# Optimization experiments

Hardware: AMD Instinct MI355X
Metric: run time of the kernel (lower is better)

The kernel has to match this reference:

```python
import jax, jax.numpy as jnp
import numpy as np

B, S, D = 2, 2048, 2048
H = 1024          # per-expert swiglu hidden
E = 16            # num_experts
K = 2             # top_k
T = B * S
CAP = (K * T) // E  # capacity = top_k * tokens / experts * capacity_factor(1.0) = 512


def setup_inputs() -> dict:
    key = jax.random.key(0)
    ks = jax.random.split(key, 10)
    s = 0.02
    return {
        "hidden_states": jax.random.normal(ks[0], (B, S, D), jnp.float32),
        "gate_w": jax.random.normal(ks[1], (D, E), jnp.float32) * s,
        "w1": jax.random.normal(ks[2], (E, D, H), jnp.float32) * s,
        "w3": jax.random.normal(ks[3], (E, D, H), jnp.float32) * s,
        "w2": jax.random.normal(ks[4], (E, H, D), jnp.float32) * s,
        "sw1": jax.random.normal(ks[5], (D, H), jnp.float32) * s,
        "sw3": jax.random.normal(ks[6], (D, H), jnp.float32) * s,
        "sw2": jax.random.normal(ks[7], (H, D), jnp.float32) * s,
        "coef_w": jax.random.normal(ks[8], (D, 2), jnp.float32) * s,
        "coef_b": jnp.zeros((2,), jnp.float32),
    }


def _topk_gating(logits):
    """GShard-style top-k capacity gating. logits: [T,E] (gate runs in fp32).
    Returns combine [T,E,C], dispatch [T,E,C], l_aux scalar, exp_counts [E]."""
    probs = jax.nn.softmax(logits, axis=-1)                     # [T,E]
    top_vals, top_idx = jax.lax.top_k(probs, K)                 # [T,K]
    gates = top_vals / jnp.sum(top_vals, -1, keepdims=True)     # renormalize top-k
    masks = jax.nn.one_hot(top_idx, E, dtype=probs.dtype)       # [T,K,E]

    prior = jnp.zeros((E,), probs.dtype)
    combine = jnp.zeros((T, E, CAP), probs.dtype)
    for kk in range(K):  # fixed tiny K, structurally distinct slots
        m = masks[:, kk]                                        # [T,E]
        loc = jnp.cumsum(m, axis=0) - m + prior                 # position in expert buffer
        prior = prior + jnp.sum(m, axis=0)
        keep = m * (loc < CAP)                                  # capacity drop
        pos = jnp.sum(loc * m, axis=1).astype(jnp.int32)        # [T]
        loc_oh = jax.nn.one_hot(pos, CAP, dtype=probs.dtype)    # [T,C]
        combine = combine + gates[:, kk, None, None] * keep[:, :, None] * loc_oh[:, None, :]
    dispatch = (combine > 0).astype(probs.dtype)

    # load-balancing aux loss over top-1 assignment (GShard/DeepSpeed convention)
    me = jnp.mean(probs, axis=0)                                # [E]
    ce = jnp.mean(masks[:, 0], axis=0)                          # [E]
    l_aux = jnp.sum(me * ce) * E
    exp_counts = jnp.sum(masks, axis=(0, 1)).astype(jnp.int32)  # tokens routed per expert
    return combine, dispatch, l_aux, exp_counts


def _swiglu(x, a, b, c):
    return (jax.nn.silu(x @ a) * (x @ b)) @ c


def reference(hidden_states, gate_w, w1, w3, w2, sw1, sw3, sw2, coef_w, coef_b):
    x = hidden_states.reshape(T, D)
    logits = (x.astype(jnp.float32) @ gate_w)                   # gate kept in fp32
    combine, dispatch, l_aux, exp_counts = _topk_gating(logits)

    # dispatch -> grouped expert swiglu -> combine
    xe = jnp.einsum('tec,td->ecd', dispatch.astype(x.dtype), x)         # [E,C,D]
    h = jax.nn.silu(jnp.einsum('ecd,edh->ech', xe, w1)) * jnp.einsum('ecd,edh->ech', xe, w3)
    ye = jnp.einsum('ech,ehd->ecd', h, w2)                              # [E,C,D]
    moe_out = jnp.einsum('tec,ecd->td', combine.astype(x.dtype), ye)    # [T,D]

    # shared-expert residual MLP + softmax coefficient combine
    mlp_out = _swiglu(x, sw1, sw3, sw2)                                 # [T,D]
    coef = jax.nn.softmax(x @ coef_w + coef_b, axis=-1)                 # [T,2]
    out = moe_out * coef[:, 0:1] + mlp_out * coef[:, 1:2]
    return out.reshape(B, S, D), l_aux, exp_counts
```

## Files before the change

kernel.cpp:

```cpp
#include <hip/hip_runtime.h>
#include <hip/hip_bf16.h>
#include <stdint.h>

#define T_TOK 4096
#define DIM   2048
#define HID   1024
#define NE    16
#define CAPE  512

typedef __bf16 bf16x8 __attribute__((ext_vector_type(8)));
typedef float  f32x4  __attribute__((ext_vector_type(4)));

__device__ __forceinline__ ushort f2bf(float f) {
    union { float f; uint32_t u; } v; v.f = f;
    uint32_t r = (v.u + 0x7FFFu + ((v.u >> 16) & 1u)) >> 16;
    return (ushort)r;
}
__device__ __forceinline__ float bf2f(ushort u) {
    union { uint32_t u; float f; } v; v.u = (uint32_t)u << 16; return v.f;
}
__device__ __forceinline__ void gload16(const void* g, void* lds) {
    __builtin_amdgcn_global_load_lds(
        (const __attribute__((address_space(1))) uint32_t*)g,
        (__attribute__((address_space(3))) uint32_t*)lds, 16, 0, 0);
}
#define VMCNT(n) asm volatile("s_waitcnt vmcnt(" #n ")" ::: "memory")

__global__ __launch_bounds__(256) void logits_kernel(
    const float* __restrict__ x, const float* __restrict__ gate_w,
    const float* __restrict__ coef_w, float* __restrict__ logits,
    ushort* __restrict__ xb)
{
    __shared__ float gws[18 * 512];
    int tid = threadIdx.x;
    int wv = tid >> 6, lane = tid & 63;
    int tbase = blockIdx.x * 16 + wv * 4;
    float acc[4][18];
#pragma unroll
    for (int tk = 0; tk < 4; ++tk)
#pragma unroll
        for (int o = 0; o < 18; ++o) acc[tk][o] = 0.f;

    for (int c = 0; c < 4; ++c) {
        int d0 = c * 512;
        __syncthreads();
        const float4* g4 = (const float4*)(gate_w + (size_t)d0 * NE);
        for (int i = tid; i < 2048; i += 256) {
            float4 v = g4[i];
            int dd = i >> 2, o0 = (i & 3) * 4;
            gws[(o0 + 0) * 512 + dd] = v.x;
            gws[(o0 + 1) * 512 + dd] = v.y;
            gws[(o0 + 2) * 512 + dd] = v.z;
            gws[(o0 + 3) * 512 + dd] = v.w;
        }
        for (int i = tid; i < 1024; i += 256) {
            float v = coef_w[(size_t)d0 * 2 + i];
            gws[(16 + (i & 1)) * 512 + (i >> 1)] = v;
        }
        __syncthreads();
#pragma unroll
        for (int tk = 0; tk < 4; ++tk) {
            int t = tbase + tk;
            const float* xr = x + (size_t)t * DIM + d0;
            float xv[8];
#pragma unroll
            for (int j = 0; j < 8; ++j) xv[j] = xr[j * 64 + lane];
#pragma unroll
            for (int j = 0; j < 8; ++j)
                xb[(size_t)t * DIM + d0 + j * 64 + lane] = f2bf(xv[j]);
#pragma unroll
            for (int o = 0; o < 18; ++o) {
                const float* gr = &gws[o * 512 + lane];
                float a = acc[tk][o];
#pragma unroll
                for (int j = 0; j < 8; ++j) a += xv[j] * gr[j * 64];
                acc[tk][o] = a;
            }
        }
    }
#pragma unroll
    for (int tk = 0; tk < 4; ++tk) {
#pragma unroll
        for (int off = 32; off > 0; off >>= 1)
#pragma unroll
            for (int o = 0; o < 18; ++o)
                acc[tk][o] += __shfl_down(acc[tk][o], off, 64);
        if (lane == 0) {
#pragma unroll
            for (int o = 0; o < 18; ++o)
                logits[(size_t)(tbase + tk) * 18 + o] = acc[tk][o];
        }
    }
}

__global__ __launch_bounds__(256) void finish_kernel(
    const float* __restrict__ logits, const float* __restrict__ coef_b,
    int* __restrict__ topidx, float* __restrict__ gatesw,
    float* __restrict__ coefo, float* __restrict__ probs_sum)
{
    __shared__ float wred[4][NE];
    int t = blockIdx.x * 256 + threadIdx.x;
    float lg[18];
#pragma unroll
    for (int o = 0; o < 18; ++o) lg[o] = logits[(size_t)t * 18 + o];
    float p[NE];
    float m = lg[0];
#pragma unroll
    for (int e = 1; e < NE; ++e) m = fmaxf(m, lg[e]);
    float ssum = 0.f;
#pragma unroll
    for (int e = 0; e < NE; ++e) { p[e] = expf(lg[e] - m); ssum += p[e]; }
    float inv = 1.f / ssum;
#pragma unroll
    for (int e = 0; e < NE; ++e) p[e] *= inv;
    int i1 = 0;
#pragma unroll
    for (int e = 1; e < NE; ++e) if (p[e] > p[i1]) i1 = e;
    int i2 = -1;
#pragma unroll
    for (int e = 0; e < NE; ++e) { if (e == i1) continue; if (i2 < 0 || p[e] > p[i2]) i2 = e; }
    float g0 = p[i1], g1 = p[i2], gs = g0 + g1;
    topidx[t * 2 + 0] = i1; topidx[t * 2 + 1] = i2;
    gatesw[t * 2 + 0] = g0 / gs; gatesw[t * 2 + 1] = g1 / gs;
    float c0 = lg[16] + coef_b[0], c1 = lg[17] + coef_b[1];
    float cm = fmaxf(c0, c1);
    float e0 = expf(c0 - cm), e1 = expf(c1 - cm);
    float cs = e0 + e1;
    coefo[t * 2 + 0] = e0 / cs; coefo[t * 2 + 1] = e1 / cs;

    float r[NE];
#pragma unroll
    for (int e = 0; e < NE; ++e) r[e] = p[e];
#pragma unroll
    for (int off = 32; off > 0; off >>= 1) {
#pragma unroll
        for (int e = 0; e < NE; ++e) r[e] += __shfl_down(r[e], off, 64);
    }
    int wv = threadIdx.x >> 6, ln = threadIdx.x & 63;
    if (ln == 0) {
#pragma unroll
        for (int e = 0; e < NE; ++e) wred[wv][e] = r[e];
    }
    __syncthreads();
    if (threadIdx.x < NE) {
        float s = wred[0][threadIdx.x] + wred[1][threadIdx.x]
                + wred[2][threadIdx.x] + wred[3][threadIdx.x];
        atomicAdd(&probs_sum[threadIdx.x], s);
    }
}

__global__ __launch_bounds__(256) void scan_kernel(
    const int* __restrict__ topidx, const float* __restrict__ gatesw,
    const float* __restrict__ probs_sum,
    int* __restrict__ sidx, float* __restrict__ swt,
    int* __restrict__ assign_token, int* __restrict__ nvalid,
    float* __restrict__ out_tail)
{
    int e = blockIdx.x;
    __shared__ int wcnt[4];
    __shared__ int runs;
    __shared__ int cnt0s;
    int tid = threadIdx.x, wv = tid >> 6, ln = tid & 63;
    unsigned long long ltmask = (1ull << ln) - 1ull;
    if (tid == 0) runs = 0;
    __syncthreads();
    for (int kk = 0; kk < 2; ++kk) {
        for (int c = 0; c < T_TOK; c += 256) {
            int t = c + tid;
            bool m = (topidx[t * 2 + kk] == e);
            unsigned long long b = __ballot(m);
            int within = __popcll(b & ltmask);
            if (ln == 0) wcnt[wv] = __popcll(b);
            __syncthreads();
            int cross = 0;
            for (int w = 0; w < wv; ++w) cross += wcnt[w];
            int pos = runs + cross + within;
            if (m) {
                bool keep = pos < CAPE;
                sidx[t * 2 + kk] = keep ? (e * CAPE + pos) : -1;
                swt[t * 2 + kk] = keep ? gatesw[t * 2 + kk] : 0.f;
                if (keep) assign_token[e * CAPE + pos] = t;
            }
            __syncthreads();
            if (tid == 0) runs += wcnt[0] + wcnt[1] + wcnt[2] + wcnt[3];
            __syncthreads();
        }
        if (kk == 0 && tid == 0) cnt0s = runs;
        __syncthreads();
    }
    for (int p = runs + tid; p < CAPE; p += 256)
        assign_token[e * CAPE + p] = 0;
    if (tid == 0) {
        int total = runs;
        nvalid[e] = min(CAPE, total);
        out_tail[1 + e] = (float)total;
        float term = (probs_sum[e] / (float)T_TOK) * ((float)cnt0s / (float)T_TOK) * (float)NE;
        atomicAdd(&out_tail[0], term);
    }
}

__global__ __launch_bounds__(256) void transpose_all(
    const float* __restrict__ w1, const float* __restrict__ w3,
    const float* __restrict__ w2, const float* __restrict__ sw1,
    const float* __restrict__ sw3, const float* __restrict__ sw2,
    ushort* __restrict__ w1T, ushort* __restrict__ w3T, ushort* __restrict__ w2T,
    ushort* __restrict__ sw1T, ushort* __restrict__ sw3T, ushort* __restrict__ sw2T)
{
    __shared__ __align__(16) ushort tile[128][264];
    int id = blockIdx.x;
    const float* in; ushort* outp; int R, C, tx, ty;
    if (id < 3072) {
        int seg = id >> 10;
        int rem = id & 1023;
        int e = rem >> 6;
        int r2 = rem & 63;
        if (seg < 2) {
            R = DIM; C = HID; tx = r2 & 7; ty = r2 >> 3;
            in   = (seg ? w3 : w1) + (size_t)e * DIM * HID;
            outp = (seg ? w3T : w1T) + (size_t)e * HID * DIM;
        } else {
            R = HID; C = DIM; tx = r2 & 3; ty = r2 >> 2;
            in   = w2 + (size_t)e * HID * DIM;
            outp = w2T + (size_t)e * DIM * HID;
        }
    } else {
        int id2 = id - 3072;
        int seg = id2 >> 6;
        int r2 = id2 & 63;
        if (seg < 2) {
            R = DIM; C = HID; tx = r2 & 7; ty = r2 >> 3;
            in = seg ? sw3 : sw1; outp = seg ? sw3T : sw1T;
        } else {
            R = HID; C = DIM; tx = r2 & 3; ty = r2 >> 2;
            in = sw2; outp = sw2T;
        }
    }
    int r0 = tx * 256, c0 = ty * 128;
    int tid = threadIdx.x;
    int t31 = tid & 31, t8 = tid >> 5;

#pragma unroll
    for (int it = 0; it < 8; ++it) {
        int r4 = (it * 8 + t8) * 4;
        int c4 = t31 * 4;
        const float* ip = in + (size_t)(r0 + r4) * C + c0 + c4;
        float va[4][4];
        *(float4*)va[0] = *(const float4*)(ip);
        *(float4*)va[1] = *(const float4*)(ip + C);
        *(float4*)va[2] = *(const float4*)(ip + 2 * (size_t)C);
        *(float4*)va[3] = *(const float4*)(ip + 3 * (size_t)C);
#pragma unroll
        for (int j = 0; j < 4; ++j) {
            uint2 u;
            u.x = (uint32_t)f2bf(va[0][j]) | ((uint32_t)f2bf(va[1][j]) << 16);
            u.y = (uint32_t)f2bf(va[2][j]) | ((uint32_t)f2bf(va[3][j]) << 16);
            *(uint2*)&tile[c4 + j][r4] = u;
        }
    }
    __syncthreads();

#pragma unroll
    for (int it = 0; it < 16; ++it) {
        int c = it * 8 + t8;
        int k = t31 * 8;
        uint4 o = *(const uint4*)&tile[c][k];
        *(uint4*)(outp + (size_t)(c0 + c) * R + r0 + k) = o;
    }
}

__device__ __forceinline__ void stage_half_off(
    const ushort* __restrict__ G, int k0, char* region, int tid,
    size_t off0, size_t off1)
{
#pragma unroll
    for (int q = 0; q < 2; ++q) {
        int c = q * 512 + tid;
        int row = c >> 3;
        int cb = (c & 7) << 4;
        int scb = cb ^ ((row & 7) << 4);
        const ushort* src = G + (q ? off1 : off0) + k0 + (scb >> 1);
        gload16(src, region + ((c - (tid & 63)) << 4));
    }
}

__device__ __forceinline__ bf16x8 ldfrag(const char* lds, int region, int row, int cb) {
    return *(const bf16x8*)(lds + region + row * 128 + (cb ^ ((row & 7) << 4)));
}

template<int NB>
__device__ __forceinline__ void core_single(
    const ushort* __restrict__ A, const ushort* __restrict__ B,
    size_t a0, size_t a1, size_t a2, size_t a3,
    size_t b0, size_t b1, size_t b2, size_t b3,
    int K, char* lds, f32x4 (&acc)[8][NB], int tid)
{
    const int DB = 32768 + NB * 8192;
    int lane = tid & 63;
    int wid = tid >> 6;
    int wrow = wid >> 2, wcol = wid & 3;
    int l15 = lane & 15, hi = lane >> 4;

#pragma unroll
    for (int m = 0; m < 8; ++m)
#pragma unroll
        for (int n = 0; n < NB; ++n)
            acc[m][n] = (f32x4){0.f, 0.f, 0.f, 0.f};

    int nj = K >> 7;

    stage_half_off(A, 0, lds + 0,           tid, a0, a1);
    stage_half_off(A, 0, lds + 16384,       tid, a2, a3);
    stage_half_off(B, 0, lds + 32768,       tid, b0, b1);
    if (NB == 4) stage_half_off(B, 0, lds + 32768 + 16384, tid, b2, b3);
    stage_half_off(B, 64, lds + DB + 32768, tid, b0, b1);
    if (NB == 4) stage_half_off(B, 64, lds + DB + 32768 + 16384, tid, b2, b3);
    if (NB == 4) VMCNT(4); else VMCNT(2);
    __builtin_amdgcn_s_barrier();
    __builtin_amdgcn_sched_barrier(0);

    for (int j = 0; j < nj; ++j) {
        int k1 = (2 * j + 1) << 6, k2 = (2 * j + 2) << 6, k3 = (2 * j + 3) << 6;
        bool st = (j < nj - 1);
#pragma unroll
        for (int d = 0; d < 2; ++d) {
            char* LA = lds + d * DB;
            char* LB = LA + 32768;
            char* LAo = lds + (d ^ 1) * DB;
            bf16x8 bf[NB][2];
#pragma unroll
            for (int p = 0; p < 4; ++p) {
                if (p == 0) {
#pragma unroll
                    for (int n = 0; n < NB; ++n)
#pragma unroll
                        for (int ks = 0; ks < 2; ++ks)
                            bf[n][ks] = ldfrag(LB, 0, wcol * (16 * NB) + n * 16 + l15, ks * 64 + hi * 16);
                }
                bf16x8 af[2][2];
#pragma unroll
                for (int i = 0; i < 2; ++i)
#pragma unroll
                    for (int ks = 0; ks < 2; ++ks)
                        af[i][ks] = ldfrag(LA, 0, wrow * 128 + (2 * p + i) * 16 + l15, ks * 64 + hi * 16);
                if (d == 0) {
                    if (p == 0)      stage_half_off(A, k1, LAo,         tid, a0, a1);
                    else if (p == 1) stage_half_off(A, k1, LAo + 16384, tid, a2, a3);
                    else if (p == 2) { if (st) stage_half_off(B, k2, LB, tid, b0, b1); }
                    else             { if (st && NB == 4) stage_half_off(B, k2, LB + 16384, tid, b2, b3); }
                } else {
                    if (st) {
                        if (p == 0)      stage_half_off(A, k2, LAo,         tid, a0, a1);
                        else if (p == 1) stage_half_off(A, k2, LAo + 16384, tid, a2, a3);
                        else if (p == 2) stage_half_off(B, k3, LB, tid, b0, b1);
                        else             { if (NB == 4) stage_half_off(B, k3, LB + 16384, tid, b2, b3); }
                    }
                }
                __builtin_amdgcn_s_barrier();
                if (p == 3) {
                    if (d == 0) {
                        if (st) { if (NB == 4) VMCNT(4); else VMCNT(2); }
                        else    VMCNT(0);
                    } else if (st) {
                        if (NB == 4) VMCNT(4); else VMCNT(2);
                    }
                }
                asm volatile("s_waitcnt lgkmcnt(0)" ::: "memory");
                __builtin_amdgcn_sched_barrier(0);
                __builtin_amdgcn_s_setprio(1);
#pragma unroll
                for (int i = 0; i < 2; ++i)
#pragma unroll
                    for (int n = 0; n < NB; ++n)
#pragma unroll
                        for (int ks = 0; ks < 2; ++ks)
                            acc[2 * p + i][n] = __builtin_amdgcn_mfma_f32_16x16x32_bf16(
                                af[i][ks], bf[n][ks], acc[2 * p + i][n], 0, 0, 0);
                __builtin_amdgcn_s_setprio(0);
                __builtin_amdgcn_s_barrier();
                __builtin_amdgcn_sched_barrier(0);
            }
        }
    }
}

template<int NM>
__device__ __forceinline__ void core_dual(
    const ushort* __restrict__ A, const ushort* __restrict__ B1,
    const ushort* __restrict__ B3,
    size_t a0, size_t a1, size_t a2, size_t a3,
    size_t b0, size_t b1,
    int K, char* lds, f32x4 (&acc1)[8][NM], f32x4 (&acc3)[8][NM], int tid)
{
    const int DB = 32768 + NM * 16384;
    int lane = tid & 63;
    int wid = tid >> 6;
    int wrow = wid >> 2, wcol = wid & 3;
    int l15 = lane & 15, hi = lane >> 4;

#pragma unroll
    for (int m = 0; m < 8; ++m)
#pragma unroll
        for (int n = 0; n < NM; ++n) {
            acc1[m][n] = (f32x4){0.f, 0.f, 0.f, 0.f};
            acc3[m][n] = (f32x4){0.f, 0.f, 0.f, 0.f};
        }

    int nj = K >> 7;

    stage_half_off(A, 0, lds + 0,     tid, a0, a1);
    stage_half_off(A, 0, lds + 16384, tid, a2, a3);
    stage_half_off(B1, 0, lds + 32768, tid, b0, b1);
    if (NM == 2) stage_half_off(B3, 0, lds + 32768 + 16384, tid, b0, b1);
    stage_half_off(B1, 64, lds + DB + 32768, tid, b0, b1);
    if (NM == 2) stage_half_off(B3, 64, lds + DB + 32768 + 16384, tid, b0, b1);
    if (NM == 2) VMCNT(4); else VMCNT(2);
    __builtin_amdgcn_s_barrier();
    __builtin_amdgcn_sched_barrier(0);

    for (int j = 0; j < nj; ++j) {
        int k1 = (2 * j + 1) << 6, k2 = (2 * j + 2) << 6, k3 = (2 * j + 3) << 6;
        bool st = (j < nj - 1);
#pragma unroll
        for (int d = 0; d < 2; ++d) {
            char* LA = lds + d * DB;
            char* LB = LA + 32768;
            char* LAo = lds + (d ^ 1) * DB;
            bf16x8 bf1[NM][2], bf3[NM][2];
#pragma unroll
            for (int p = 0; p < 4; ++p) {
                if (p == 0) {
#pragma unroll
                    for (int n = 0; n < NM; ++n)
#pragma unroll
                        for (int ks = 0; ks < 2; ++ks) {
                            int brow = wcol * (16 * NM) + n * 16 + l15;
                            bf1[n][ks] = ldfrag(LB, 0, brow,           ks * 64 + hi * 16);
                            bf3[n][ks] = ldfrag(LB, 0, brow + NM * 64, ks * 64 + hi * 16);
                        }
                }
                bf16x8 af[2][2];
#pragma unroll
                for (int i = 0; i < 2; ++i)
#pragma unroll
                    for (int ks = 0; ks < 2; ++ks)
                        af[i][ks] = ldfrag(LA, 0, wrow * 128 + (2 * p + i) * 16 + l15, ks * 64 + hi * 16);
                if (d == 0) {
                    if (p == 0)      stage_half_off(A, k1, LAo,         tid, a0, a1);
                    else if (p == 1) stage_half_off(A, k1, LAo + 16384, tid, a2, a3);
                    else if (p == 2) { if (st) stage_half_off(B1, k2, LB, tid, b0, b1); }
                    else             { if (st && NM == 2) stage_half_off(B3, k2, LB + 16384, tid, b0, b1); }
                } else {
                    if (st) {
                        if (p == 0)      stage_half_off(A, k2, LAo,         tid, a0, a1);
                        else if (p == 1) stage_half_off(A, k2, LAo + 16384, tid, a2, a3);
                        else if (p == 2) stage_half_off(B1, k3, LB, tid, b0, b1);
                        else             { if (NM == 2) stage_half_off(B3, k3, LB + 16384, tid, b0, b1); }
                    }
                }
                __builtin_amdgcn_s_barrier();
                if (p == 3) {
                    if (d == 0) {
                        if (st) { if (NM == 2) VMCNT(4); else VMCNT(2); }
                        else    VMCNT(0);
                    } else if (st) {
                        if (NM == 2) VMCNT(4); else VMCNT(2);
                    }
                }
                asm volatile("s_waitcnt lgkmcnt(0)" ::: "memory");
                __builtin_amdgcn_sched_barrier(0);
                __builtin_amdgcn_s_setprio(1);
#pragma unroll
                for (int i = 0; i < 2; ++i)
#pragma unroll
                    for (int n = 0; n < NM; ++n)
#pragma unroll
                        for (int ks = 0; ks < 2; ++ks) {
                            acc1[2 * p + i][n] = __builtin_amdgcn_mfma_f32_16x16x32_bf16(
                                af[i][ks], bf1[n][ks], acc1[2 * p + i][n], 0, 0, 0);
                            acc3[2 * p + i][n] = __builtin_amdgcn_mfma_f32_16x16x32_bf16(
                                af[i][ks], bf3[n][ks], acc3[2 * p + i][n], 0, 0, 0);
                        }
                __builtin_amdgcn_s_setprio(0);
                __builtin_amdgcn_s_barrier();
                __builtin_amdgcn_sched_barrier(0);
            }
        }
    }
}

__global__ __launch_bounds__(512, 2) void gemm8_up(
    const ushort* __restrict__ xb,
    const ushort* __restrict__ w1T, const ushort* __restrict__ w3T,
    const ushort* __restrict__ sw1T, const ushort* __restrict__ sw3T,
    const int* __restrict__ assign_token,
    ushort* __restrict__ HH, const int* __restrict__ nvalid)
{
    __shared__ __align__(16) char lds[131072];
    int b = blockIdx.x;
    int tid = threadIdx.x;
    int rr = tid >> 3;
    int lane = tid & 63, wid = tid >> 6;
    int wrow = wid >> 2, wcol = wid & 3;

    if (b < 256) {
        int id = (b & 7) * 32 + (b >> 3);
        int e = id >> 4, rem = id & 15;
        int mt = rem >> 3, nt = rem & 7;
        int bm = mt * 256, bn = nt * 128;
        if (bm >= nvalid[e]) return;
        const int* at = assign_token + e * CAPE + bm;
        size_t a0 = (size_t)at[rr] * DIM;
        size_t a1 = (size_t)at[64 + rr] * DIM;
        size_t a2 = (size_t)at[128 + rr] * DIM;
        size_t a3 = (size_t)at[192 + rr] * DIM;
        const ushort* B1 = w1T + (size_t)e * HID * DIM;
        const ushort* B3 = w3T + (size_t)e * HID * DIM;
        size_t b0 = (size_t)(bn + rr) * DIM;
        size_t b1 = (size_t)(bn + 64 + rr) * DIM;
        f32x4 acc1[8][2], acc3[8][2];
        core_dual<2>(xb, B1, B3, a0, a1, a2, a3, b0, b1, DIM, lds, acc1, acc3, tid);
        ushort* O = HH + (size_t)e * CAPE * HID;
        int rbase = bm + wrow * 128 + (lane >> 4) * 4;
        int cbase = bn + wcol * 32 + (lane & 15);
#pragma unroll
        for (int m = 0; m < 8; ++m)
#pragma unroll
            for (int n = 0; n < 2; ++n) {
                int col = cbase + n * 16;
#pragma unroll
                for (int r = 0; r < 4; ++r) {
                    float g = acc1[m][n][r];
                    float s = g / (1.f + __expf(-g));
                    O[(size_t)(rbase + m * 16 + r) * HID + col] = f2bf(s * acc3[m][n][r]);
                }
            }
    } else {
        int b2 = b - 256;
        int id = (b2 & 7) * 32 + (b2 >> 3);
        int mt = id >> 4, nt = id & 15;
        int bm = mt * 256, bn = nt * 64;
        size_t a0 = (size_t)(bm + rr) * DIM;
        size_t a1 = (size_t)(bm + 64 + rr) * DIM;
        size_t a2 = (size_t)(bm + 128 + rr) * DIM;
        size_t a3 = (size_t)(bm + 192 + rr) * DIM;
        size_t b0 = (size_t)(bn + rr) * DIM;
        size_t b1 = (size_t)(sw3T - sw1T) + (size_t)(bn + rr) * DIM;
        f32x4 acc1[8][1], acc3[8][1];
        core_dual<1>(xb, sw1T, sw1T, a0, a1, a2, a3, b0, b1, DIM, lds, acc1, acc3, tid);
        ushort* O = HH + (size_t)NE * CAPE * HID;
        int rbase = bm + wrow * 128 + (lane >> 4) * 4;
        int col = bn + wcol * 16 + (lane & 15);
#pragma unroll
        for (int m = 0; m < 8; ++m)
#pragma unroll
            for (int r = 0; r < 4; ++r) {
                float g = acc1[m][0][r];
                float s = g / (1.f + __expf(-g));
                O[(size_t)(rbase + m * 16 + r) * HID + col] = f2bf(s * acc3[m][0][r]);
            }
    }
}

__global__ __launch_bounds__(512, 2) void gemm8_down(
    const ushort* __restrict__ HH, const ushort* __restrict__ w2T,
    const ushort* __restrict__ sw2T, ushort* __restrict__ ye,
    float* __restrict__ outp, const float* __restrict__ coefo,
    const int* __restrict__ nvalid)
{
    __shared__ __align__(16) char lds[131072];
    int b = blockIdx.x;
    int tid = threadIdx.x;
    int rr = tid >> 3;
    int lane = tid & 63, wid = tid >> 6;
    int wrow = wid >> 2, wcol = wid & 3;

    if (b < 256) {
        int id = (b & 7) * 32 + (b >> 3);
        int e = id >> 4, rem = id & 15;
        int mt = rem >> 3, nt = rem & 7;
        int bm = mt * 256, bn = nt * 256;
        if (bm >= nvalid[e]) return;
        const ushort* A = HH + (size_t)e * CAPE * HID;
        const ushort* B = w2T + (size_t)e * DIM * HID;
        ushort* Ob = ye + (size_t)e * CAPE * DIM;
        size_t a0 = (size_t)(bm + rr) * HID;
        size_t a1 = (size_t)(bm + 64 + rr) * HID;
        size_t a2 = (size_t)(bm + 128 + rr) * HID;
        size_t a3 = (size_t)(bm + 192 + rr) * HID;
        size_t b0 = (size_t)(bn + rr) * HID;
        size_t b1 = (size_t)(bn + 64 + rr) * HID;
        size_t b2 = (size_t)(bn + 128 + rr) * HID;
        size_t b3 = (size_t)(bn + 192 + rr) * HID;
        f32x4 acc[8][4];
        core_single<4>(A, B, a0, a1, a2, a3, b0, b1, b2, b3, HID, lds, acc, tid);
        int rbase = bm + wrow * 128 + (lane >> 4) * 4;
        int cbase = bn + wcol * 64 + (lane & 15);
#pragma unroll
        for (int m = 0; m < 8; ++m)
#pragma unroll
            for (int n = 0; n < 4; ++n) {
                int col = cbase + n * 16;
#pragma unroll
                for (int r = 0; r < 4; ++r)
                    Ob[(size_t)(rbase + m * 16 + r) * DIM + col] = f2bf(acc[m][n][r]);
            }
    } else {
        int b2i = b - 256;
        int id = (b2i & 7) * 32 + (b2i >> 3);
        int mt = id >> 4, nt = id & 15;
        int bm = mt * 256, bn = nt * 128;
        const ushort* A = HH + (size_t)NE * CAPE * HID;
        const ushort* B = sw2T;
        size_t a0 = (size_t)(bm + rr) * HID;
        size_t a1 = (size_t)(bm + 64 + rr) * HID;
        size_t a2 = (size_t)(bm + 128 + rr) * HID;
        size_t a3 = (size_t)(bm + 192 + rr) * HID;
        size_t b0 = (size_t)(bn + rr) * HID;
        size_t b1 = (size_t)(bn + 64 + rr) * HID;
        f32x4 acc[8][2];
        core_single<2>(A, B, a0, a1, a2, a3, b0, b1, 0, 0, HID, lds, acc, tid);
        int rbase = bm + wrow * 128 + (lane >> 4) * 4;
        int cbase = bn + wcol * 32 + (lane & 15);
#pragma unroll
        for (int m = 0; m < 8; ++m)
#pragma unroll
            for (int n = 0; n < 2; ++n) {
                int col = cbase + n * 16;
#pragma unroll
                for (int r = 0; r < 4; ++r) {
                    int row = rbase + m * 16 + r;
                    outp[(size_t)row * DIM + col] = acc[m][n][r] * coefo[2 * row + 1];
                }
            }
    }
}

__global__ __launch_bounds__(256) void combine_kernel(
    const ushort* __restrict__ ye, const int* __restrict__ sidx,
    const float* __restrict__ swt, const float* __restrict__ coefo,
    float* __restrict__ out)
{
    int idx = blockIdx.x * 256 + threadIdx.x;
    int t = idx >> 9;
    int d = (idx & 511) << 2;
    int s0 = sidx[t * 2], s1 = sidx[t * 2 + 1];
    float c0 = coefo[t * 2];
    float w0 = swt[t * 2] * c0, w1 = swt[t * 2 + 1] * c0;
    float4 v = *(float4*)(out + (size_t)t * DIM + d);
    if (s0 >= 0) {
        uint2 y = *(const uint2*)(ye + (size_t)s0 * DIM + d);
        const ushort* yp = (const ushort*)&y;
        v.x += w0 * bf2f(yp[0]); v.y += w0 * bf2f(yp[1]);
        v.z += w0 * bf2f(yp[2]); v.w += w0 * bf2f(yp[3]);
    }
    if (s1 >= 0) {
        uint2 y = *(const uint2*)(ye + (size_t)s1 * DIM + d);
        const ushort* yp = (const ushort*)&y;
        v.x += w1 * bf2f(yp[0]); v.y += w1 * bf2f(yp[1]);
        v.z += w1 * bf2f(yp[2]); v.w += w1 * bf2f(yp[3]);
    }
    *(float4*)(out + (size_t)t * DIM + d) = v;
}

extern "C" void kernel_launch(void* const* d_in, const int* in_sizes, int n_in,
                              void* d_out, int out_size, void* d_ws, size_t ws_size,
                              hipStream_t stream)
{
    const float* x      = (const float*)d_in[0];
    const float* gate_w = (const float*)d_in[1];
    const float* w1     = (const float*)d_in[2];
    const float* w3     = (const float*)d_in[3];
    const float* w2     = (const float*)d_in[4];
    const float* sw1    = (const float*)d_in[5];
    const float* sw3    = (const float*)d_in[6];
    const float* sw2    = (const float*)d_in[7];
    const float* coef_w = (const float*)d_in[8];
    const float* coef_b = (const float*)d_in[9];
    float* out = (float*)d_out;

    char* ws = (char*)d_ws;
    size_t off = 0;
    auto alloc = [&](size_t bytes) -> void* {
        void* p = ws + off;
        off += (bytes + 255) & ~(size_t)255;
        return p;
    };
    float*  probs_sum    = (float*)alloc(NE * 4);
    int*    nvalid       = (int*)alloc(NE * 4);
    int*    topidx       = (int*)alloc((size_t)T_TOK * 2 * 4);
    float*  gatesw       = (float*)alloc((size_t)T_TOK * 2 * 4);
    float*  coefo        = (float*)alloc((size_t)T_TOK * 2 * 4);
    int*    sidx         = (int*)alloc((size_t)T_TOK * 2 * 4);
    float*  swt          = (float*)alloc((size_t)T_TOK * 2 * 4);
    int*    assign_token = (int*)alloc((size_t)NE * CAPE * 4);
    float*  logits       = (float*)alloc((size_t)T_TOK * 18 * 4);
    ushort* w1T  = (ushort*)alloc((size_t)NE * HID * DIM * 2);
    ushort* w3T  = (ushort*)alloc((size_t)NE * HID * DIM * 2);
    ushort* w2T  = (ushort*)alloc((size_t)NE * DIM * HID * 2);
    ushort* sw1T = (ushort*)alloc((size_t)HID * DIM * 2);
    ushort* sw3T = (ushort*)alloc((size_t)HID * DIM * 2);
    ushort* sw2T = (ushort*)alloc((size_t)DIM * HID * 2);
    ushort* xb   = (ushort*)alloc((size_t)T_TOK * DIM * 2);
    size_t HROWS = (size_t)NE * CAPE + T_TOK;
    ushort* HH   = (ushort*)alloc(HROWS * HID * 2);
    ushort* ye   = (ushort*)alloc((size_t)NE * CAPE * DIM * 2);

    hipMemsetAsync(probs_sum, 0, NE * 4, stream);
    hipMemsetAsync(out + (size_t)T_TOK * DIM, 0, 4, stream);

    logits_kernel<<<T_TOK / 16, 256, 0, stream>>>(x, gate_w, coef_w, logits, xb);
    finish_kernel<<<T_TOK / 256, 256, 0, stream>>>(logits, coef_b,
                                                   topidx, gatesw, coefo, probs_sum);
    scan_kernel<<<NE, 256, 0, stream>>>(topidx, gatesw, probs_sum,
                                        sidx, swt, assign_token, nvalid,
                                        out + (size_t)T_TOK * DIM);

    transpose_all<<<3264, 256, 0, stream>>>(w1, w3, w2, sw1, sw3, sw2,
                                            w1T, w3T, w2T, sw1T, sw3T, sw2T);

    gemm8_up<<<512, 512, 0, stream>>>(xb, w1T, w3T, sw1T, sw3T, assign_token, HH, nvalid);
    gemm8_down<<<512, 512, 0, stream>>>(HH, w2T, sw2T, ye, out, coefo, nvalid);

    combine_kernel<<<(T_TOK * (DIM / 4)) / 256, 256, 0, stream>>>(ye, sidx, swt, coefo, out);
}
```

Baseline: 402.9 us.

## Fuse gating into logits kernel, merge scan with transpose, stage MLP output in bf16

The softmax/top-2/coef computation moves into the logits kernel's epilogue, which removes the finish kernel and the logits buffer. Per-block probability partials replace the atomic accumulation and the memsets. The scan now runs as extra blocks inside the weight-transpose launch, so the two kernels run concurrently. The shared-expert down-projection writes a bf16 buffer instead of fp32 into out, which halves that write and read in combine at some precision cost.

```diff
diff --git a/kernel.cpp b/kernel.cpp
--- a/kernel.cpp
+++ b/kernel.cpp
@@ -28,10 +28,14 @@
 
 __global__ __launch_bounds__(256) void logits_kernel(
     const float* __restrict__ x, const float* __restrict__ gate_w,
-    const float* __restrict__ coef_w, float* __restrict__ logits,
-    ushort* __restrict__ xb)
+    const float* __restrict__ coef_w, const float* __restrict__ coef_b,
+    ushort* __restrict__ xb,
+    int* __restrict__ topidx, float* __restrict__ gatesw,
+    float* __restrict__ coefo, float* __restrict__ probs_part,
+    float* __restrict__ laux)
 {
     __shared__ float gws[18 * 512];
+    __shared__ float wred[4][NE];
     int tid = threadIdx.x;
     int wv = tid >> 6, lane = tid & 63;
     int tbase = blockIdx.x * 16 + wv * 4;
@@ -79,127 +83,66 @@
         }
     }
 #pragma unroll
-    for (int tk = 0; tk < 4; ++tk) {
+    for (int tk = 0; tk < 4; ++tk)
 #pragma unroll
         for (int off = 32; off > 0; off >>= 1)
 #pragma unroll
             for (int o = 0; o < 18; ++o)
                 acc[tk][o] += __shfl_down(acc[tk][o], off, 64);
-        if (lane == 0) {
-#pragma unroll
-            for (int o = 0; o < 18; ++o)
-                logits[(size_t)(tbase + tk) * 18 + o] = acc[tk][o];
-        }
-    }
-}
-
-__global__ __launch_bounds__(256) void finish_kernel(
-    const float* __restrict__ logits, const float* __restrict__ coef_b,
-    int* __restrict__ topidx, float* __restrict__ gatesw,
-    float* __restrict__ coefo, float* __restrict__ probs_sum)
-{
-    __shared__ float wred[4][NE];
-    int t = blockIdx.x * 256 + threadIdx.x;
-    float lg[18];
-#pragma unroll
-    for (int o = 0; o < 18; ++o) lg[o] = logits[(size_t)t * 18 + o];
-    float p[NE];
-    float m = lg[0];
-#pragma unroll
-    for (int e = 1; e < NE; ++e) m = fmaxf(m, lg[e]);
-    float ssum = 0.f;
-#pragma unroll
-    for (int e = 0; e < NE; ++e) { p[e] = expf(lg[e] - m); ssum += p[e]; }
-    float inv = 1.f / ssum;
-#pragma unroll
-    for (int e = 0; e < NE; ++e) p[e] *= inv;
-    int i1 = 0;
-#pragma unroll
-    for (int e = 1; e < NE; ++e) if (p[e] > p[i1]) i1 = e;
-    int i2 = -1;
-#pragma unroll
-    for (int e = 0; e < NE; ++e) { if (e == i1) continue; if (i2 < 0 || p[e] > p[i2]) i2 = e; }
-    float g0 = p[i1], g1 = p[i2], gs = g0 + g1;
-    topidx[t * 2 + 0] = i1; topidx[t * 2 + 1] = i2;
-    gatesw[t * 2 + 0] = g0 / gs; gatesw[t * 2 + 1] = g1 / gs;
-    float c0 = lg[16] + coef_b[0], c1 = lg[17] + coef_b[1];
-    float cm = fmaxf(c0, c1);
-    float e0 = expf(c0 - cm), e1 = expf(c1 - cm);
-    float cs = e0 + e1;
-    coefo[t * 2 + 0] = e0 / cs; coefo[t * 2 + 1] = e1 / cs;
-
-    float r[NE];
-#pragma unroll
-    for (int e = 0; e < NE; ++e) r[e] = p[e];
-#pragma unroll
-    for (int off = 32; off > 0; off >>= 1) {
-#pragma unroll
-        for (int e = 0; e < NE; ++e) r[e] += __shfl_down(r[e], off, 64);
-    }
-    int wv = threadIdx.x >> 6, ln = threadIdx.x & 63;
-    if (ln == 0) {
-#pragma unroll
-        for (int e = 0; e < NE; ++e) wred[wv][e] = r[e];
+
+    if (lane == 0) {
+        float ps[NE];
+#pragma unroll
+        for (int e = 0; e < NE; ++e) ps[e] = 0.f;
+#pragma unroll
+        for (int tk = 0; tk < 4; ++tk) {
+            int t = tbase + tk;
+            float lg[18];
+#pragma unroll
+            for (int o = 0; o < 18; ++o) lg[o] = acc[tk][o];
+            float m = lg[0];
+#pragma unroll
+            for (int e = 1; e < NE; ++e) m = fmaxf(m, lg[e]);
+            float p[NE];
+            float ssum = 0.f;
+#pragma unroll
+            for (int e = 0; e < NE; ++e) { p[e] = expf(lg[e] - m); ssum += p[e]; }
+            float inv = 1.f / ssum;
+#pragma unroll
+            for (int e = 0; e < NE; ++e) p[e] *= inv;
+            int i1 = 0;
+#pragma unroll
+            for (int e = 1; e < NE; ++e) if (p[e] > p[i1]) i1 = e;
+            int i2 = -1;
+#pragma unroll
+            for (int e = 0; e < NE; ++e) { if (e == i1) continue; if (i2 < 0 || p[e] > p[i2]) i2 = e; }
+            float g0 = p[i1], g1 = p[i2], gs = g0 + g1;
+            topidx[t * 2 + 0] = i1; topidx[t * 2 + 1] = i2;
+            gatesw[t * 2 + 0] = g0 / gs; gatesw[t * 2 + 1] = g1 / gs;
+            float c0 = lg[16] + coef_b[0], c1 = lg[17] + coef_b[1];
+            float cm = fmaxf(c0, c1);
+            float e0 = expf(c0 - cm), e1 = expf(c1 - cm);
+            float cs = e0 + e1;
+            coefo[t * 2 + 0] = e0 / cs; coefo[t * 2 + 1] = e1 / cs;
+#pragma unroll
+            for (int e = 0; e < NE; ++e) ps[e] += p[e];
+        }
+#pragma unroll
+        for (int e = 0; e < NE; ++e) wred[wv][e] = ps[e];
     }
     __syncthreads();
-    if (threadIdx.x < NE) {
-        float s = wred[0][threadIdx.x] + wred[1][threadIdx.x]
-                + wred[2][threadIdx.x] + wred[3][threadIdx.x];
-        atomicAdd(&probs_sum[threadIdx.x], s);
-    }
-}
-
-__global__ __launch_bounds__(256) void scan_kernel(
+    if (tid < NE)
+        probs_part[blockIdx.x * NE + tid] =
+            wred[0][tid] + wred[1][tid] + wred[2][tid] + wred[3][tid];
+    if (blockIdx.x == 0 && tid == 0) laux[0] = 0.f;
+}
+
+__global__ __launch_bounds__(256) void scan_transpose(
     const int* __restrict__ topidx, const float* __restrict__ gatesw,
-    const float* __restrict__ probs_sum,
+    const float* __restrict__ probs_part,
     int* __restrict__ sidx, float* __restrict__ swt,
     int* __restrict__ assign_token, int* __restrict__ nvalid,
-    float* __restrict__ out_tail)
-{
-    int e = blockIdx.x;
-    __shared__ int wcnt[4];
-    __shared__ int runs;
-    __shared__ int cnt0s;
-    int tid = threadIdx.x, wv = tid >> 6, ln = tid & 63;
-    unsigned long long ltmask = (1ull << ln) - 1ull;
-    if (tid == 0) runs = 0;
-    __syncthreads();
-    for (int kk = 0; kk < 2; ++kk) {
-        for (int c = 0; c < T_TOK; c += 256) {
-            int t = c + tid;
-            bool m = (topidx[t * 2 + kk] == e);
-            unsigned long long b = __ballot(m);
-            int within = __popcll(b & ltmask);
-            if (ln == 0) wcnt[wv] = __popcll(b);
-            __syncthreads();
-            int cross = 0;
-            for (int w = 0; w < wv; ++w) cross += wcnt[w];
-            int pos = runs + cross + within;
-            if (m) {
-                bool keep = pos < CAPE;
-                sidx[t * 2 + kk] = keep ? (e * CAPE + pos) : -1;
-                swt[t * 2 + kk] = keep ? gatesw[t * 2 + kk] : 0.f;
-                if (keep) assign_token[e * CAPE + pos] = t;
-            }
-            __syncthreads();
-            if (tid == 0) runs += wcnt[0] + wcnt[1] + wcnt[2] + wcnt[3];
-            __syncthreads();
-        }
-        if (kk == 0 && tid == 0) cnt0s = runs;
-        __syncthreads();
-    }
-    for (int p = runs + tid; p < CAPE; p += 256)
-        assign_token[e * CAPE + p] = 0;
-    if (tid == 0) {
-        int total = runs;
-        nvalid[e] = min(CAPE, total);
-        out_tail[1 + e] = (float)total;
-        float term = (probs_sum[e] / (float)T_TOK) * ((float)cnt0s / (float)T_TOK) * (float)NE;
-        atomicAdd(&out_tail[0], term);
-    }
-}
-
-__global__ __launch_bounds__(256) void transpose_all(
+    float* __restrict__ out_tail,
     const float* __restrict__ w1, const float* __restrict__ w3,
     const float* __restrict__ w2, const float* __restrict__ sw1,
     const float* __restrict__ sw3, const float* __restrict__ sw2,
@@ -207,7 +150,61 @@
     ushort* __restrict__ sw1T, ushort* __restrict__ sw3T, ushort* __restrict__ sw2T)
 {
     __shared__ __align__(16) ushort tile[128][264];
-    int id = blockIdx.x;
+    int tid = threadIdx.x;
+
+    if (blockIdx.x < NE) {
+        __shared__ int wcnt[4];
+        __shared__ float fred[4];
+        __shared__ int runs;
+        __shared__ int cnt0s;
+        int e = blockIdx.x;
+        int wv = tid >> 6, ln = tid & 63;
+        unsigned long long ltmask = (1ull << ln) - 1ull;
+        if (tid == 0) runs = 0;
+        __syncthreads();
+        for (int kk = 0; kk < 2; ++kk) {
+            for (int c = 0; c < T_TOK; c += 256) {
+                int t = c + tid;
+                bool m = (topidx[t * 2 + kk] == e);
+                unsigned long long b = __ballot(m);
+                int within = __popcll(b & ltmask);
+                if (ln == 0) wcnt[wv] = __popcll(b);
+                __syncthreads();
+                int cross = 0;
+                for (int w = 0; w < wv; ++w) cross += wcnt[w];
+                int pos = runs + cross + within;
+                if (m) {
+                    bool keep = pos < CAPE;
+                    sidx[t * 2 + kk] = keep ? (e * CAPE + pos) : -1;
+                    swt[t * 2 + kk] = keep ? gatesw[t * 2 + kk] : 0.f;
+                    if (keep) assign_token[e * CAPE + pos] = t;
+                }
+                __syncthreads();
+                if (tid == 0) runs += wcnt[0] + wcnt[1] + wcnt[2] + wcnt[3];
+                __syncthreads();
+            }
+            if (kk == 0 && tid == 0) cnt0s = runs;
+            __syncthreads();
+        }
+        for (int p = runs + tid; p < CAPE; p += 256)
+            assign_token[e * CAPE + p] = 0;
+        float val = probs_part[tid * NE + e];
+#pragma unroll
+        for (int off = 32; off > 0; off >>= 1) val += __shfl_down(val, off, 64);
+        if (ln == 0) fred[wv] = val;
+        __syncthreads();
+        if (tid == 0) {
+            float psum = fred[0] + fred[1] + fred[2] + fred[3];
+            int total = runs;
+            nvalid[e] = min(CAPE, total);
+            out_tail[1 + e] = (float)total;
+            float term = (psum / (float)T_TOK) * ((float)cnt0s / (float)T_TOK) * (float)NE;
+            atomicAdd(&out_tail[0], term);
+        }
+        return;
+    }
+
+    int id = blockIdx.x - NE;
     const float* in; ushort* outp; int R, C, tx, ty;
     if (id < 3072) {
         int seg = id >> 10;
@@ -236,7 +233,6 @@
         }
     }
     int r0 = tx * 256, c0 = ty * 128;
-    int tid = threadIdx.x;
     int t31 = tid & 31, t8 = tid >> 5;
 
 #pragma unroll
@@ -564,7 +560,7 @@
 __global__ __launch_bounds__(512, 2) void gemm8_down(
     const ushort* __restrict__ HH, const ushort* __restrict__ w2T,
     const ushort* __restrict__ sw2T, ushort* __restrict__ ye,
-    float* __restrict__ outp, const float* __restrict__ coefo,
+    ushort* __restrict__ mlpb, const float* __restrict__ coefo,
     const int* __restrict__ nvalid)
 {
     __shared__ __align__(16) char lds[131072];
@@ -629,16 +625,16 @@
 #pragma unroll
                 for (int r = 0; r < 4; ++r) {
                     int row = rbase + m * 16 + r;
-                    outp[(size_t)row * DIM + col] = acc[m][n][r] * coefo[2 * row + 1];
+                    mlpb[(size_t)row * DIM + col] = f2bf(acc[m][n][r] * coefo[2 * row + 1]);
                 }
             }
     }
 }
 
 __global__ __launch_bounds__(256) void combine_kernel(
-    const ushort* __restrict__ ye, const int* __restrict__ sidx,
-    const float* __restrict__ swt, const float* __restrict__ coefo,
-    float* __restrict__ out)
+    const ushort* __restrict__ ye, const ushort* __restrict__ mlpb,
+    const int* __restrict__ sidx, const float* __restrict__ swt,
+    const float* __restrict__ coefo, float* __restrict__ out)
 {
     int idx = blockIdx.x * 256 + threadIdx.x;
     int t = idx >> 9;
@@ -646,7 +642,10 @@
     int s0 = sidx[t * 2], s1 = sidx[t * 2 + 1];
     float c0 = coefo[t * 2];
     float w0 = swt[t * 2] * c0, w1 = swt[t * 2 + 1] * c0;
-    float4 v = *(float4*)(out + (size_t)t * DIM + d);
+    uint2 mb = *(const uint2*)(mlpb + (size_t)t * DIM + d);
+    const ushort* mp = (const ushort*)&mb;
+    float4 v;
+    v.x = bf2f(mp[0]); v.y = bf2f(mp[1]); v.z = bf2f(mp[2]); v.w = bf2f(mp[3]);
     if (s0 >= 0) {
         uint2 y = *(const uint2*)(ye + (size_t)s0 * DIM + d);
         const ushort* yp = (const ushort*)&y;
@@ -685,7 +684,6 @@
         off += (bytes + 255) & ~(size_t)255;
         return p;
     };
-    float*  probs_sum    = (float*)alloc(NE * 4);
     int*    nvalid       = (int*)alloc(NE * 4);
     int*    topidx       = (int*)alloc((size_t)T_TOK * 2 * 4);
     float*  gatesw       = (float*)alloc((size_t)T_TOK * 2 * 4);
@@ -693,7 +691,7 @@
     int*    sidx         = (int*)alloc((size_t)T_TOK * 2 * 4);
     float*  swt          = (float*)alloc((size_t)T_TOK * 2 * 4);
     int*    assign_token = (int*)alloc((size_t)NE * CAPE * 4);
-    float*  logits       = (float*)alloc((size_t)T_TOK * 18 * 4);
+    float*  probs_part   = (float*)alloc((size_t)256 * NE * 4);
     ushort* w1T  = (ushort*)alloc((size_t)NE * HID * DIM * 2);
     ushort* w3T  = (ushort*)alloc((size_t)NE * HID * DIM * 2);
     ushort* w2T  = (ushort*)alloc((size_t)NE * DIM * HID * 2);
@@ -704,22 +702,17 @@
     size_t HROWS = (size_t)NE * CAPE + T_TOK;
     ushort* HH   = (ushort*)alloc(HROWS * HID * 2);
     ushort* ye   = (ushort*)alloc((size_t)NE * CAPE * DIM * 2);
-
-    hipMemsetAsync(probs_sum, 0, NE * 4, stream);
-    hipMemsetAsync(out + (size_t)T_TOK * DIM, 0, 4, stream);
-
-    logits_kernel<<<T_TOK / 16, 256, 0, stream>>>(x, gate_w, coef_w, logits, xb);
-    finish_kernel<<<T_TOK / 256, 256, 0, stream>>>(logits, coef_b,
-                                                   topidx, gatesw, coefo, probs_sum);
-    scan_kernel<<<NE, 256, 0, stream>>>(topidx, gatesw, probs_sum,
-                                        sidx, swt, assign_token, nvalid,
-                                        out + (size_t)T_TOK * DIM);
-
-    transpose_all<<<3264, 256, 0, stream>>>(w1, w3, w2, sw1, sw3, sw2,
-                                            w1T, w3T, w2T, sw1T, sw3T, sw2T);
-
+    ushort* mlpb = (ushort*)alloc((size_t)T_TOK * DIM * 2);
+
+    float* out_tail = out + (size_t)T_TOK * DIM;
+
+    logits_kernel<<<T_TOK / 16, 256, 0, stream>>>(
+        x, gate_w, coef_w, coef_b, xb, topidx, gatesw, coefo, probs_part, out_tail);
+    scan_transpose<<<NE + 3264, 256, 0, stream>>>(
+        topidx, gatesw, probs_part, sidx, swt, assign_token, nvalid, out_tail,
+        w1, w3, w2, sw1, sw3, sw2, w1T, w3T, w2T, sw1T, sw3T, sw2T);
     gemm8_up<<<512, 512, 0, stream>>>(xb, w1T, w3T, sw1T, sw3T, assign_token, HH, nvalid);
-    gemm8_down<<<512, 512, 0, stream>>>(HH, w2T, sw2T, ye, out, coefo, nvalid);
-
-    combine_kernel<<<(T_TOK * (DIM / 4)) / 256, 256, 0, stream>>>(ye, sidx, swt, coefo, out);
-}
+    gemm8_down<<<512, 512, 0, stream>>>(HH, w2T, sw2T, ye, mlpb, coefo, nvalid);
+    combine_kernel<<<(T_TOK * (DIM / 4)) / 256, 256, 0, stream>>>(
+        ye, mlpb, sidx, swt, coefo, out);
+}
```

New measurement: 400.5 us. Within noise of the previous version (-0.6%).
